# Performance work log

Hardware: AMD Instinct MI355X
Metric: run time of the kernel (lower is better)

The kernel has to match this reference:

```python
import jax, jax.numpy as jnp
import numpy as np

# Dimensions (see shape_source)
IN_VEC = 131072          # input_vector_size
NUM_CAPS = 512           # num_capsules (output capsules)
CAP_SIZE = 256           # capsule_size
RF_SIZE = 64             # receptive_field_size
RF_PER_CAP = CAP_SIZE // RF_SIZE        # 4
IN_CAPS = IN_VEC // CAP_SIZE            # 512 input_eff_capsules
CONN_P = 0.1             # connection_probability


def setup_inputs() -> dict:
    key = jax.random.key(0)
    kx, kc, kw = jax.random.split(key, 3)
    x = jax.random.normal(kx, (IN_VEC,), dtype=jnp.float32)
    # Sparse ScRRAMBLe routing tensor: mostly zeros, gated by connection probability.
    # Shape (input_eff_capsules, rf_per_cap_in, num_capsules, rf_per_cap_out) per einsum 'ijkl,ijm->klm'.
    Ci = (jax.random.uniform(kc, (IN_CAPS, RF_PER_CAP, NUM_CAPS, RF_PER_CAP)) < CONN_P).astype(jnp.float32)
    # glorot_normal over last two axes: fan_in = fan_out = RF_SIZE -> std = sqrt(2/(64+64)) = 0.125
    glorot_std = float(np.sqrt(2.0 / (RF_SIZE + RF_SIZE)))
    Wi = glorot_std * jax.random.normal(kw, (NUM_CAPS, RF_PER_CAP, RF_PER_CAP, RF_SIZE, RF_SIZE), dtype=jnp.float32)
    return {"x": x, "Ci": Ci, "Wi": Wi}


def reference(x, Ci, Wi):
    # x: (IN_VEC,) -> (input_eff_capsules, rf_per_cap, rf_size)
    x_reshaped = x.reshape(IN_CAPS, RF_PER_CAP, RF_SIZE)
    # Route input receptive fields to output capsule slots:
    # x_routed: (num_capsules, rf_per_cap, rf_size)
    x_routed = jnp.einsum('ijkl,ijm->klm', Ci, x_reshaped)
    # Per-capsule small batched transform:
    # y: (num_capsules, rf_per_cap, rf_size)
    y = jnp.einsum('ijklm,ikm->ijl', Wi, x_routed)
    return y
```

## Files before the change

kernel.cpp:

```cpp
#include <hip/hip_runtime.h>


typedef float f4 __attribute__((ext_vector_type(4)));

__global__ __launch_bounds__(256, 2) void fused_caps_kernel(
    const float* __restrict__ x,
    const float* __restrict__ Ci,
    const float* __restrict__ Wi,
    float* __restrict__ y)
{
    const int c    = blockIdx.x;
    const int t    = threadIdx.x;
    const int w    = t >> 6;
    const int lane = t & 63;
    const int lq   = lane >> 4;
    const int m16  = lane & 15;

    const f4* __restrict__ Ci4 = (const f4*)Ci;
    const f4* __restrict__ W4  = (const f4*)Wi;

    __shared__ f4    ci_s[2048];
    __shared__ float part[4 * 4 * 64];

    {
        f4 cv[8];
        #pragma unroll
        for (int u = 0; u < 8; ++u)
            cv[u] = Ci4[(t + (u << 8)) * 512 + c];
        #pragma unroll
        for (int u = 0; u < 8; ++u)
            ci_s[t + (u << 8)] = cv[u];
    }
    __syncthreads();

    f4 acc = {0.f, 0.f, 0.f, 0.f};
    {
        const int ij0 = w << 9;
        const float* __restrict__ xp = x + lane;
        for (int it = 0; it < 512; it += 16) {
            float xv[16];
            #pragma unroll
            for (int u = 0; u < 16; ++u)
                xv[u] = xp[(ij0 + it + u) << 6];
            #pragma unroll
            for (int u = 0; u < 16; ++u)
                acc += ci_s[ij0 + it + u] * xv[u];
        }
    }
    part[(w << 8) +   0 + lane] = acc.x;
    part[(w << 8) +  64 + lane] = acc.y;
    part[(w << 8) + 128 + lane] = acc.z;
    part[(w << 8) + 192 + lane] = acc.w;
    __syncthreads();

    const f4* partf4 = (const f4*)part;
    f4 xr0 = partf4[  0 + m16] + partf4[ 64 + m16] + partf4[128 + m16] + partf4[192 + m16];
    f4 xr1 = partf4[ 16 + m16] + partf4[ 80 + m16] + partf4[144 + m16] + partf4[208 + m16];
    f4 xr2 = partf4[ 32 + m16] + partf4[ 96 + m16] + partf4[160 + m16] + partf4[224 + m16];
    f4 xr3 = partf4[ 48 + m16] + partf4[112 + m16] + partf4[176 + m16] + partf4[240 + m16];

    const int wbase = ((c << 2) + w) << 12;

    f4 wvA[16], wvB[16];

#define PREFETCH(dst, g4)                                                   \
    _Pragma("unroll")                                                       \
    for (int c2 = 0; c2 < 4; ++c2) {                                        \
        const int l = ((g4) << 4) + (c2 << 2) + lq;                         \
        _Pragma("unroll")                                                   \
        for (int k = 0; k < 4; ++k)                                         \
            dst[(c2 << 2) + k] =                                            \
                __builtin_nontemporal_load(&W4[wbase + (k << 10) + l * 16 + m16]); \
    }

#define COMPUTE(src, g4)                                                    \
    _Pragma("unroll")                                                       \
    for (int c2 = 0; c2 < 4; ++c2) {                                        \
        f4 s = src[(c2 << 2) + 0] * xr0 + src[(c2 << 2) + 1] * xr1          \
             + src[(c2 << 2) + 2] * xr2 + src[(c2 << 2) + 3] * xr3;         \
        float p = s.x + s.y + s.z + s.w;                                    \
        p += __shfl_xor(p, 1);                                              \
        p += __shfl_xor(p, 2);                                              \
        p += __shfl_xor(p, 4);                                              \
        p += __shfl_xor(p, 8);                                              \
        if (m16 == 0)                                                       \
            y[(((c << 2) + w) << 6) + ((g4) << 4) + (c2 << 2) + lq] = p;    \
    }

    PREFETCH(wvA, 0)
    PREFETCH(wvB, 1)
    COMPUTE(wvA, 0)
    PREFETCH(wvA, 2)
    COMPUTE(wvB, 1)
    PREFETCH(wvB, 3)
    COMPUTE(wvA, 2)
    COMPUTE(wvB, 3)

#undef PREFETCH
#undef COMPUTE
}

extern "C" void kernel_launch(void* const* d_in, const int* in_sizes, int n_in,
                              void* d_out, int out_size, void* d_ws, size_t ws_size,
                              hipStream_t stream) {
    const float* x  = (const float*)d_in[0];
    const float* Ci = (const float*)d_in[1];
    const float* Wi = (const float*)d_in[2];
    float* y = (float*)d_out;

    fused_caps_kernel<<<512, 256, 0, stream>>>(x, Ci, Wi, y);
}
```

Baseline: 224.5 us.

## Stream Wi through LDS with async global_load_lds double buffering

Replaces the register-prefetched Wi loads with direct global-to-LDS asynchronous loads (global_load_lds, 16 bytes) into per-wave double buffers, using explicit vmcnt waits to pipeline eight smaller stages. The aim is to free registers held by the 32 f4 prefetch buffers and to keep more memory requests in flight while computing. LDS is enlarged to 64KB and shared between Ci staging, partial sums and W buffers, with an added barrier. The larger LDS footprint may limit occupancy, and the per-wave buffers can be reused without intra-wave sync safety guarantees.

Measured after the change: 232.6 us. 1.04x slower.

```diff
diff --git a/kernel.cpp b/kernel.cpp
--- a/kernel.cpp
+++ b/kernel.cpp
@@ -2,6 +2,13 @@
 
 
 typedef float f4 __attribute__((ext_vector_type(4)));
+
+#define GLDS16(gsrc, ldst)                                                   \
+    __builtin_amdgcn_global_load_lds(                                        \
+        (const __attribute__((address_space(1))) unsigned int*)(gsrc),       \
+        (__attribute__((address_space(3))) unsigned int*)(ldst), 16, 0, 0)
+
+#define VMW(n) asm volatile("s_waitcnt vmcnt(" #n ")" ::: "memory")
 
 __global__ __launch_bounds__(256, 2) void fused_caps_kernel(
     const float* __restrict__ x,
@@ -17,10 +24,11 @@
     const int m16  = lane & 15;
 
     const f4* __restrict__ Ci4 = (const f4*)Ci;
-    const f4* __restrict__ W4  = (const f4*)Wi;
 
-    __shared__ f4    ci_s[2048];
-    __shared__ float part[4 * 4 * 64];
+    __shared__ f4 lds[4096];
+
+    f4*    ci_s  = lds + 256;
+    float* partf = (float*)lds;
 
     {
         f4 cv[8];
@@ -47,56 +55,63 @@
                 acc += ci_s[ij0 + it + u] * xv[u];
         }
     }
-    part[(w << 8) +   0 + lane] = acc.x;
-    part[(w << 8) +  64 + lane] = acc.y;
-    part[(w << 8) + 128 + lane] = acc.z;
-    part[(w << 8) + 192 + lane] = acc.w;
+    partf[(w << 8) +   0 + lane] = acc.x;
+    partf[(w << 8) +  64 + lane] = acc.y;
+    partf[(w << 8) + 128 + lane] = acc.z;
+    partf[(w << 8) + 192 + lane] = acc.w;
     __syncthreads();
 
-    const f4* partf4 = (const f4*)part;
+    const f4* partf4 = (const f4*)partf;
     f4 xr0 = partf4[  0 + m16] + partf4[ 64 + m16] + partf4[128 + m16] + partf4[192 + m16];
     f4 xr1 = partf4[ 16 + m16] + partf4[ 80 + m16] + partf4[144 + m16] + partf4[208 + m16];
     f4 xr2 = partf4[ 32 + m16] + partf4[ 96 + m16] + partf4[160 + m16] + partf4[224 + m16];
     f4 xr3 = partf4[ 48 + m16] + partf4[112 + m16] + partf4[176 + m16] + partf4[240 + m16];
+    __syncthreads();
 
-    const int wbase = ((c << 2) + w) << 12;
+    const float* __restrict__ WfB = Wi + ((size_t)((c << 2) + w) << 14);
 
-    f4 wvA[16], wvB[16];
-
-#define PREFETCH(dst, g4)                                                   \
-    _Pragma("unroll")                                                       \
-    for (int c2 = 0; c2 < 4; ++c2) {                                        \
-        const int l = ((g4) << 4) + (c2 << 2) + lq;                         \
-        _Pragma("unroll")                                                   \
-        for (int k = 0; k < 4; ++k)                                         \
-            dst[(c2 << 2) + k] =                                            \
-                __builtin_nontemporal_load(&W4[wbase + (k << 10) + l * 16 + m16]); \
+#define STAGE(buf, tt)                                                       \
+    _Pragma("unroll")                                                        \
+    for (int k = 0; k < 4; ++k) {                                            \
+        _Pragma("unroll")                                                    \
+        for (int c2b = 0; c2b < 2; ++c2b) {                                  \
+            const int l = (((tt) >> 1) << 4) + (((tt) & 1) << 3)             \
+                        + (c2b << 2) + lq;                                   \
+            GLDS16(WfB + (k << 12) + (l << 6) + (m16 << 2),                  \
+                   &lds[(w << 10) + ((buf) << 9) + (((k << 1) + c2b) << 6)]);\
+        }                                                                    \
     }
 
-#define COMPUTE(src, g4)                                                    \
-    _Pragma("unroll")                                                       \
-    for (int c2 = 0; c2 < 4; ++c2) {                                        \
-        f4 s = src[(c2 << 2) + 0] * xr0 + src[(c2 << 2) + 1] * xr1          \
-             + src[(c2 << 2) + 2] * xr2 + src[(c2 << 2) + 3] * xr3;         \
-        float p = s.x + s.y + s.z + s.w;                                    \
-        p += __shfl_xor(p, 1);                                              \
-        p += __shfl_xor(p, 2);                                              \
-        p += __shfl_xor(p, 4);                                              \
-        p += __shfl_xor(p, 8);                                              \
-        if (m16 == 0)                                                       \
-            y[(((c << 2) + w) << 6) + ((g4) << 4) + (c2 << 2) + lq] = p;    \
+#define COMPUTE(buf, tt)                                                     \
+    _Pragma("unroll")                                                        \
+    for (int c2b = 0; c2b < 2; ++c2b) {                                      \
+        const f4* tb = lds + (w << 10) + ((buf) << 9);                       \
+        f4 s = tb[((0 << 1) + c2b) * 64 + lane] * xr0                        \
+             + tb[((1 << 1) + c2b) * 64 + lane] * xr1                        \
+             + tb[((2 << 1) + c2b) * 64 + lane] * xr2                        \
+             + tb[((3 << 1) + c2b) * 64 + lane] * xr3;                       \
+        float p = s.x + s.y + s.z + s.w;                                     \
+        p += __shfl_xor(p, 1);                                               \
+        p += __shfl_xor(p, 2);                                               \
+        p += __shfl_xor(p, 4);                                               \
+        p += __shfl_xor(p, 8);                                               \
+        if (m16 == 0)                                                        \
+            y[(((c << 2) + w) << 6) + (((tt) >> 1) << 4)                     \
+              + (((tt) & 1) << 3) + (c2b << 2) + lq] = p;                    \
     }
 
-    PREFETCH(wvA, 0)
-    PREFETCH(wvB, 1)
-    COMPUTE(wvA, 0)
-    PREFETCH(wvA, 2)
-    COMPUTE(wvB, 1)
-    PREFETCH(wvB, 3)
-    COMPUTE(wvA, 2)
-    COMPUTE(wvB, 3)
+    STAGE(0, 0)
+    STAGE(1, 1)
+    VMW(8); COMPUTE(0, 0) STAGE(0, 2)
+    VMW(8); COMPUTE(1, 1) STAGE(1, 3)
+    VMW(8); COMPUTE(0, 2) STAGE(0, 4)
+    VMW(8); COMPUTE(1, 3) STAGE(1, 5)
+    VMW(8); COMPUTE(0, 4) STAGE(0, 6)
+    VMW(8); COMPUTE(1, 5) STAGE(1, 7)
+    VMW(8); COMPUTE(0, 6)
+    VMW(0); COMPUTE(1, 7)
 
-#undef PREFETCH
+#undef STAGE
 #undef COMPUTE
 }
 
```
